# Kernel optimization log

Measured on AMD Instinct MI355X. Metric: run time of the kernel, lower is better.

The kernel has to match this reference:

```python
import jax, jax.numpy as jnp
import numpy as np

BN_EPS = 1e-5

def _bn(x, p):
    # p rows: gamma, beta, running_mean, running_var (eval-mode BatchNorm1d)
    g, b, m, v = p[0], p[1], p[2], p[3]
    return (x - m) * jax.lax.rsqrt(v + BN_EPS) * g + b

def setup_inputs() -> dict:
    key = jax.random.key(0)
    ks = iter(jax.random.split(key, 32))
    B, P, T, E, H = 16, 64, 8, 64, 64
    batch = B * P
    def w(shape, scale=0.1):
        return (jax.random.normal(next(ks), shape, dtype=jnp.float32) * scale)
    def bn_pack(d):
        k1, k2, k3, k4 = jax.random.split(next(ks), 4)
        gamma = 1.0 + 0.1 * jax.random.normal(k1, (d,), dtype=jnp.float32)
        beta = 0.1 * jax.random.normal(k2, (d,), dtype=jnp.float32)
        mean = 0.1 * jax.random.normal(k3, (d,), dtype=jnp.float32)
        var = 0.5 + jax.random.uniform(k4, (d,), dtype=jnp.float32)
        return jnp.stack([gamma, beta, mean, var], axis=0)
    return {
        "h_states": w((1, batch, H), 1.0),
        "end_pos": w((batch, 2), 1.0),
        "vx": w((T, batch), 1.0),
        "vy": w((T, batch), 1.0),
        "agent_type": jax.random.uniform(next(ks), (T, batch, 1), dtype=jnp.float32),
        "ws_w": w((2, E)), "ws_b": w((E,)),
        "wv_w": w((2, E)), "wv_b": w((E,)),
        "wa_w": w((6, E)), "wa_b": w((E,)),
        "att1_w": w((E, 1024)), "att1_b": w((1024,)), "att_bn1": bn_pack(1024),
        "att2_w": w((1024, 1)), "att2_b": w((1,)), "att_bn2": bn_pack(1),
        "pre1_w": w((E + H, 512)), "pre1_b": w((512,)), "pre_bn1": bn_pack(512),
        "pre2_w": w((512, 1024)), "pre2_b": w((1024,)), "pre_bn2": bn_pack(1024),
        "num_ped": P,
    }

def reference(h_states, end_pos, vx, vy, agent_type,
              ws_w, ws_b, wv_w, wv_b, wa_w, wa_b,
              att1_w, att1_b, att_bn1, att2_w, att2_b, att_bn2,
              pre1_w, pre1_b, pre_bn1, pre2_w, pre2_b, pre_bn2,
              num_ped):
    P = num_ped
    batch = end_pos.shape[0]
    B = batch // P  # uniform groups (seq_start_end = [(b*P, (b+1)*P)])
    H = h_states.shape[-1]
    h = h_states.reshape(batch, H).reshape(B, P, H)            # curr_hidden per group
    pos = end_pos.reshape(B, P, 2)
    # k = i*P + j: repeated row = pos[j], 'transposed' row = pos[i]
    rel = pos[:, None, :, :] - pos[:, :, None, :]               # [B, i, j, 2]
    rel_emb = rel @ ws_w + ws_b                                 # [B, i, j, E]
    # attention_mlp: Linear->BN->ReLU->Linear->BN->ReLU (make_mlp applies BN+act after every layer)
    a1 = jax.nn.relu(_bn(rel_emb @ att1_w + att1_b, att_bn1))   # [B, i, j, 1024]
    scores = jax.nn.relu(_bn(a1 @ att2_w + att2_b, att_bn2))    # [B, i, j, 1]
    # torch.softmax(scores, dim=1) on shape (n*n, 1): softmax over a singleton -> all ones
    aw = jax.nn.softmax(scores, axis=-1)
    # velocity embedding: computed in the original then discarded (dead code, kept for fidelity)
    vel = jnp.stack([vx[-1].reshape(B, P), vy[-1].reshape(B, P)], axis=-1)
    _vel_emb = vel @ wv_w + wv_b  # noqa: F841 (unused, matches original)
    # curr_agent_type.repeat(num_ped, 6): row k=i*P+j -> type[j] tiled to 6 features
    at6 = jnp.repeat(agent_type[0].reshape(B, P, 1), 6, axis=-1)  # [B, j, 6]
    at_emb = at6 @ wa_w + wa_b                                    # [B, j, E]
    feat_j = jnp.concatenate([h, at_emb], axis=-1)                # [B, j, H+E]
    weighted = jnp.broadcast_to(feat_j[:, None, :, :], (B, P, P, feat_j.shape[-1])) * (0.05 * aw)
    p1 = jax.nn.relu(_bn(weighted @ pre1_w + pre1_b, pre_bn1))    # [B, i, j, 512]
    p2 = jax.nn.relu(_bn(p1 @ pre2_w + pre2_b, pre_bn2))          # [B, i, j, 1024]
    pool = p2.max(axis=2)                                         # view(n,n,-1).max(1): max over j
    return pool.reshape(batch, -1)
```

## Files before the change

### kernel.cpp

```cpp
#include <hip/hip_runtime.h>
#include <hip/hip_bf16.h>

#define BN_EPS 1e-5f

typedef float f32x4 __attribute__((ext_vector_type(4)));
typedef __bf16 bfx8 __attribute__((ext_vector_type(8)));


__global__ __launch_bounds__(256) void k0_prep(
    const float* __restrict__ w2,
    const float* __restrict__ w1,
    const float* __restrict__ wa_w,
    const float* __restrict__ wa_b,
    __bf16* __restrict__ w2t,
    float* __restrict__ u_ws,
    float* __restrict__ v_ws)
{
    const int t = threadIdx.x;
    if (blockIdx.x < 128) {
        __shared__ float tile[64][69];
        const int bt  = blockIdx.x;
        const int kt0 = (bt & 7) * 64;
        const int n0  = (bt >> 3) * 64;
        #pragma unroll
        for (int i = 0; i < 4; ++i) {
            const int idx = t + i * 256;
            const int kk  = idx >> 4;
            const int nq  = (idx & 15) * 4;
            const f32x4 val = *(const f32x4*)&w2[(kt0 + kk) * 1024 + n0 + nq];
            #pragma unroll
            for (int j = 0; j < 4; ++j) tile[kk][nq + j] = val[j];
        }
        __syncthreads();
        #pragma unroll
        for (int i = 0; i < 2; ++i) {
            const int idx = t + i * 256;
            const int n   = idx >> 3;
            const int kq  = (idx & 7) * 8;
            bfx8 o;
            #pragma unroll
            for (int j = 0; j < 8; ++j) o[j] = (__bf16)tile[kq + j][n];
            *(bfx8*)&w2t[(n0 + n) * 512 + kt0 + kq] = o;
        }
    } else {
        __shared__ float Sl[64], Wbl[64];
        __shared__ float redu[4][64], redv[4][64];
        const int bu = blockIdx.x - 128;
        if (t < 64) {
            float s = 0.f;
            #pragma unroll
            for (int q = 0; q < 6; ++q) s += wa_w[q * 64 + t];
            Sl[t]  = s;
            Wbl[t] = wa_b[t];
        }
        __syncthreads();
        const int cl   = t & 63;
        const int eseg = t >> 6;
        const int c    = bu * 64 + cl;
        float pu = 0.f, pv = 0.f;
        for (int e = eseg * 16; e < eseg * 16 + 16; ++e) {
            const float w = w1[(64 + e) * 512 + c];
            pu = fmaf(Sl[e], w, pu);
            pv = fmaf(Wbl[e], w, pv);
        }
        redu[eseg][cl] = pu;
        redv[eseg][cl] = pv;
        __syncthreads();
        if (t < 64) {
            u_ws[bu * 64 + t] = redu[0][t] + redu[1][t] + redu[2][t] + redu[3][t];
            v_ws[bu * 64 + t] = redv[0][t] + redv[1][t] + redv[2][t] + redv[3][t];
        }
    }
}

__global__ __launch_bounds__(256) void k1_p1(
    const float* __restrict__ h,
    const float* __restrict__ at,
    const float* __restrict__ w1,
    const float* __restrict__ b1,
    const float* __restrict__ bn1,
    const float* __restrict__ u,
    const float* __restrict__ v,
    __bf16* __restrict__ p1b)
{
    __shared__ float x[4][64];
    const int r0 = blockIdx.x * 4;
    const int t  = threadIdx.x;
    x[t >> 6][t & 63] = 0.05f * h[(r0 + (t >> 6)) * 64 + (t & 63)];
    __syncthreads();

    float acc0[4] = {0.f, 0.f, 0.f, 0.f};
    float acc1[4] = {0.f, 0.f, 0.f, 0.f};
    #pragma unroll 8
    for (int k = 0; k < 64; ++k) {
        const float w0 = w1[k * 512 + t];
        const float wB = w1[k * 512 + t + 256];
        #pragma unroll
        for (int rr = 0; rr < 4; ++rr) {
            const float xv = x[rr][k];
            acc0[rr] = fmaf(xv, w0, acc0[rr]);
            acc1[rr] = fmaf(xv, wB, acc1[rr]);
        }
    }

    float at4[4];
    #pragma unroll
    for (int rr = 0; rr < 4; ++rr) at4[rr] = at[r0 + rr];

    #pragma unroll
    for (int which = 0; which < 2; ++which) {
        const int c = t + which * 256;
        const float uu = 0.05f * u[c];
        const float vv = fmaf(0.05f, v[c], b1[c]);
        const float g  = bn1[c];
        const float be = bn1[512 + c];
        const float mu = bn1[1024 + c];
        const float vr = bn1[1536 + c];
        const float s  = rsqrtf(vr + BN_EPS) * g;
        const float* acc = which ? acc1 : acc0;
        #pragma unroll
        for (int rr = 0; rr < 4; ++rr) {
            const float pre = acc[rr] + fmaf(at4[rr], uu, vv);
            const float val = fmaxf((pre - mu) * s + be, 0.0f);
            p1b[(r0 + rr) * 512 + c] = (__bf16)val;
        }
    }
}

__global__ __launch_bounds__(512) void k2_p2_pool(
    const __bf16* __restrict__ p1b,
    const __bf16* __restrict__ w2t,
    const float* __restrict__ b2,
    const float* __restrict__ bn2,
    float* __restrict__ out)
{
    const int cc = blockIdx.x;
    const int b  = blockIdx.y;
    const int t  = threadIdx.x;

    __shared__ __bf16 A_lds[64][136];
    __shared__ __bf16 B_lds[64][136];
    __shared__ float  red[4][64];

    const int wid  = t >> 6;
    const int lane = t & 63;
    const int mw   = wid >> 1;
    const int nw   = wid & 1;
    const int m0   = mw * 16;
    const int n0   = nw * 32;
    const int l15  = lane & 15;
    const int lhi  = lane >> 4;

    f32x4 acc[2] = {};

    for (int kt = 0; kt < 512; kt += 128) {
        #pragma unroll
        for (int i = 0; i < 2; ++i) {
            const int idx = t + i * 512;
            const int row = idx >> 4;
            const int kq  = (idx & 15) * 8;
            *(f32x4*)&A_lds[row][kq] =
                *(const f32x4*)&p1b[(b * 64 + row) * 512 + kt + kq];
            *(f32x4*)&B_lds[row][kq] =
                *(const f32x4*)&w2t[(cc * 64 + row) * 512 + kt + kq];
        }
        __syncthreads();

        #pragma unroll
        for (int ks = 0; ks < 4; ++ks) {
            const bfx8 a = *(const bfx8*)&A_lds[m0 + l15][ks * 32 + lhi * 8];
            #pragma unroll
            for (int f = 0; f < 2; ++f) {
                const bfx8 bb = *(const bfx8*)&B_lds[n0 + f * 16 + l15][ks * 32 + lhi * 8];
                acc[f] = __builtin_amdgcn_mfma_f32_16x16x32_bf16(a, bb, acc[f], 0, 0, 0);
            }
        }
        __syncthreads();
    }

    #pragma unroll
    for (int f = 0; f < 2; ++f) {
        const int cg   = cc * 64 + n0 + f * 16 + l15;
        const float s  = rsqrtf(bn2[3072 + cg] + BN_EPS) * bn2[cg];
        const float be = bn2[1024 + cg];
        const float mu = bn2[2048 + cg];
        const float bias = b2[cg];
        float mm = 0.f;
        #pragma unroll
        for (int r = 0; r < 3 + 1; ++r) {
            const float val = (acc[f][r] + bias - mu) * s + be;
            mm = fmaxf(mm, fmaxf(val, 0.f));
        }
        mm = fmaxf(mm, __shfl_xor(mm, 16));
        mm = fmaxf(mm, __shfl_xor(mm, 32));
        if (lane < 16) red[mw][n0 + f * 16 + lane] = mm;
    }
    __syncthreads();

    const int cl   = t & 63;
    const int iseg = t >> 6;
    const float pool = fmaxf(fmaxf(red[0][cl], red[1][cl]),
                             fmaxf(red[2][cl], red[3][cl]));
    const int ob = (b * 64 + iseg * 8) * 1024 + cc * 64 + cl;
    #pragma unroll
    for (int ii = 0; ii < 8; ++ii) out[ob + ii * 1024] = pool;
}

extern "C" void kernel_launch(void* const* d_in, const int* in_sizes, int n_in,
                              void* d_out, int out_size, void* d_ws, size_t ws_size,
                              hipStream_t stream) {
    const float* h    = (const float*)d_in[0];
    const float* at   = (const float*)d_in[4];
    const float* wa_w = (const float*)d_in[9];
    const float* wa_b = (const float*)d_in[10];
    const float* w1   = (const float*)d_in[17];
    const float* b1   = (const float*)d_in[18];
    const float* bn1  = (const float*)d_in[19];
    const float* w2   = (const float*)d_in[20];
    const float* b2   = (const float*)d_in[21];
    const float* bn2  = (const float*)d_in[22];

    char* ws = (char*)d_ws;
    __bf16* p1b = (__bf16*)ws;
    __bf16* w2t = (__bf16*)(ws + (1 << 20));
    float*  u   = (float*)(ws + (2 << 20));
    float*  v   = u + 512;
    float*  out = (float*)d_out;

    k0_prep<<<136, 256, 0, stream>>>(w2, w1, wa_w, wa_b, w2t, u, v);
    k1_p1<<<256, 256, 0, stream>>>(h, at, w1, b1, bn1, u, v, p1b);
    k2_p2_pool<<<dim3(16, 16), 512, 0, stream>>>(p1b, w2t, b2, bn2, out);
}
```

Before: 21.53 us.

## Fuse first MLP layer into pooled second GEMM kernel using MFMA

Merges the p1 computation into the p2+pool kernel. Each block now builds a bf16 64x128 input tile (scaled hidden plus agent-type embedding) and runs the first layer with bf16 MFMA against a transposed bf16 w1. The resulting p1 tile stays in LDS instead of going through global memory. The full 512-deep w2 slice is loaded into LDS in one pass, with its global loads issued early and held in registers. This removes one kernel launch and the p1 global round trip. In exchange, every column-chunk block recomputes layer 1 redundantly (16x duplication), LDS use is much larger, and layer 1 loses precision because its inputs are now bf16.

```diff
diff --git a/kernel.cpp b/kernel.cpp
--- a/kernel.cpp
+++ b/kernel.cpp
@@ -8,192 +8,193 @@
 
 
 __global__ __launch_bounds__(256) void k0_prep(
-    const float* __restrict__ w2,
-    const float* __restrict__ w1,
+    const float* __restrict__ w2, const float* __restrict__ w1,
+    __bf16* __restrict__ w2t, __bf16* __restrict__ w1t)
+{
+    __shared__ float tile[64][69];
+    const int t = threadIdx.x;
+    int kt0, n0, src_ld, dst_ld;
+    const float* src;
+    __bf16* dst;
+    if (blockIdx.x < 128) {
+        kt0 = (blockIdx.x & 7) * 64;  n0 = (blockIdx.x >> 3) * 64;
+        src = w2; src_ld = 1024; dst = w2t; dst_ld = 512;
+    } else {
+        const int bt = blockIdx.x - 128;
+        kt0 = (bt & 1) * 64;  n0 = (bt >> 1) * 64;
+        src = w1; src_ld = 512; dst = w1t; dst_ld = 128;
+    }
+    #pragma unroll
+    for (int i = 0; i < 4; ++i) {
+        const int idx = t + i * 256;
+        const int kk  = idx >> 4;
+        const int nq  = (idx & 15) * 4;
+        const f32x4 val = *(const f32x4*)&src[(size_t)(kt0 + kk) * src_ld + n0 + nq];
+        #pragma unroll
+        for (int j = 0; j < 4; ++j) tile[kk][nq + j] = val[j];
+    }
+    __syncthreads();
+    #pragma unroll
+    for (int i = 0; i < 2; ++i) {
+        const int idx = t + i * 256;
+        const int n   = idx >> 3;
+        const int kq  = (idx & 7) * 8;
+        bfx8 o;
+        #pragma unroll
+        for (int j = 0; j < 8; ++j) o[j] = (__bf16)tile[kq + j][n];
+        *(bfx8*)&dst[(size_t)(n0 + n) * dst_ld + kt0 + kq] = o;
+    }
+}
+
+__global__ __launch_bounds__(512, 2) void kmain(
+    const float* __restrict__ h,
+    const float* __restrict__ at,
     const float* __restrict__ wa_w,
     const float* __restrict__ wa_b,
-    __bf16* __restrict__ w2t,
-    float* __restrict__ u_ws,
-    float* __restrict__ v_ws)
-{
-    const int t = threadIdx.x;
-    if (blockIdx.x < 128) {
-        __shared__ float tile[64][69];
-        const int bt  = blockIdx.x;
-        const int kt0 = (bt & 7) * 64;
-        const int n0  = (bt >> 3) * 64;
-        #pragma unroll
-        for (int i = 0; i < 4; ++i) {
-            const int idx = t + i * 256;
-            const int kk  = idx >> 4;
-            const int nq  = (idx & 15) * 4;
-            const f32x4 val = *(const f32x4*)&w2[(kt0 + kk) * 1024 + n0 + nq];
-            #pragma unroll
-            for (int j = 0; j < 4; ++j) tile[kk][nq + j] = val[j];
-        }
-        __syncthreads();
-        #pragma unroll
-        for (int i = 0; i < 2; ++i) {
-            const int idx = t + i * 256;
-            const int n   = idx >> 3;
-            const int kq  = (idx & 7) * 8;
-            bfx8 o;
-            #pragma unroll
-            for (int j = 0; j < 8; ++j) o[j] = (__bf16)tile[kq + j][n];
-            *(bfx8*)&w2t[(n0 + n) * 512 + kt0 + kq] = o;
-        }
-    } else {
-        __shared__ float Sl[64], Wbl[64];
-        __shared__ float redu[4][64], redv[4][64];
-        const int bu = blockIdx.x - 128;
-        if (t < 64) {
-            float s = 0.f;
-            #pragma unroll
-            for (int q = 0; q < 6; ++q) s += wa_w[q * 64 + t];
-            Sl[t]  = s;
-            Wbl[t] = wa_b[t];
-        }
-        __syncthreads();
-        const int cl   = t & 63;
-        const int eseg = t >> 6;
-        const int c    = bu * 64 + cl;
-        float pu = 0.f, pv = 0.f;
-        for (int e = eseg * 16; e < eseg * 16 + 16; ++e) {
-            const float w = w1[(64 + e) * 512 + c];
-            pu = fmaf(Sl[e], w, pu);
-            pv = fmaf(Wbl[e], w, pv);
-        }
-        redu[eseg][cl] = pu;
-        redv[eseg][cl] = pv;
-        __syncthreads();
-        if (t < 64) {
-            u_ws[bu * 64 + t] = redu[0][t] + redu[1][t] + redu[2][t] + redu[3][t];
-            v_ws[bu * 64 + t] = redv[0][t] + redv[1][t] + redv[2][t] + redv[3][t];
-        }
-    }
-}
-
-__global__ __launch_bounds__(256) void k1_p1(
-    const float* __restrict__ h,
-    const float* __restrict__ at,
-    const float* __restrict__ w1,
+    const __bf16* __restrict__ w1t,
     const float* __restrict__ b1,
     const float* __restrict__ bn1,
-    const float* __restrict__ u,
-    const float* __restrict__ v,
-    __bf16* __restrict__ p1b)
-{
-    __shared__ float x[4][64];
-    const int r0 = blockIdx.x * 4;
-    const int t  = threadIdx.x;
-    x[t >> 6][t & 63] = 0.05f * h[(r0 + (t >> 6)) * 64 + (t & 63)];
-    __syncthreads();
-
-    float acc0[4] = {0.f, 0.f, 0.f, 0.f};
-    float acc1[4] = {0.f, 0.f, 0.f, 0.f};
-    #pragma unroll 8
-    for (int k = 0; k < 64; ++k) {
-        const float w0 = w1[k * 512 + t];
-        const float wB = w1[k * 512 + t + 256];
-        #pragma unroll
-        for (int rr = 0; rr < 4; ++rr) {
-            const float xv = x[rr][k];
-            acc0[rr] = fmaf(xv, w0, acc0[rr]);
-            acc1[rr] = fmaf(xv, wB, acc1[rr]);
-        }
-    }
-
-    float at4[4];
-    #pragma unroll
-    for (int rr = 0; rr < 4; ++rr) at4[rr] = at[r0 + rr];
-
-    #pragma unroll
-    for (int which = 0; which < 2; ++which) {
-        const int c = t + which * 256;
-        const float uu = 0.05f * u[c];
-        const float vv = fmaf(0.05f, v[c], b1[c]);
-        const float g  = bn1[c];
-        const float be = bn1[512 + c];
-        const float mu = bn1[1024 + c];
-        const float vr = bn1[1536 + c];
-        const float s  = rsqrtf(vr + BN_EPS) * g;
-        const float* acc = which ? acc1 : acc0;
-        #pragma unroll
-        for (int rr = 0; rr < 4; ++rr) {
-            const float pre = acc[rr] + fmaf(at4[rr], uu, vv);
-            const float val = fmaxf((pre - mu) * s + be, 0.0f);
-            p1b[(r0 + rr) * 512 + c] = (__bf16)val;
-        }
-    }
-}
-
-__global__ __launch_bounds__(512) void k2_p2_pool(
-    const __bf16* __restrict__ p1b,
     const __bf16* __restrict__ w2t,
     const float* __restrict__ b2,
     const float* __restrict__ bn2,
     float* __restrict__ out)
 {
-    const int cc = blockIdx.x;
-    const int b  = blockIdx.y;
-    const int t  = threadIdx.x;
-
-    __shared__ __bf16 A_lds[64][136];
-    __shared__ __bf16 B_lds[64][136];
-    __shared__ float  red[4][64];
-
+    const int cc   = blockIdx.x;
+    const int b    = blockIdx.y;
+    const int t    = threadIdx.x;
     const int wid  = t >> 6;
     const int lane = t & 63;
-    const int mw   = wid >> 1;
-    const int nw   = wid & 1;
-    const int m0   = mw * 16;
-    const int n0   = nw * 32;
     const int l15  = lane & 15;
     const int lhi  = lane >> 4;
 
-    f32x4 acc[2] = {};
-
-    for (int kt = 0; kt < 512; kt += 128) {
-        #pragma unroll
-        for (int i = 0; i < 2; ++i) {
-            const int idx = t + i * 512;
-            const int row = idx >> 4;
-            const int kq  = (idx & 15) * 8;
-            *(f32x4*)&A_lds[row][kq] =
-                *(const f32x4*)&p1b[(b * 64 + row) * 512 + kt + kq];
-            *(f32x4*)&B_lds[row][kq] =
-                *(const f32x4*)&w2t[(cc * 64 + row) * 512 + kt + kq];
-        }
-        __syncthreads();
-
-        #pragma unroll
-        for (int ks = 0; ks < 4; ++ks) {
-            const bfx8 a = *(const bfx8*)&A_lds[m0 + l15][ks * 32 + lhi * 8];
-            #pragma unroll
-            for (int f = 0; f < 2; ++f) {
-                const bfx8 bb = *(const bfx8*)&B_lds[n0 + f * 16 + l15][ks * 32 + lhi * 8];
-                acc[f] = __builtin_amdgcn_mfma_f32_16x16x32_bf16(a, bb, acc[f], 0, 0, 0);
+    __shared__ __bf16 x_lds[64][136];
+    __shared__ __bf16 p1_lds[64][520];
+    __shared__ __bf16 B2_lds[64][520];
+    __shared__ float  red[4][64];
+
+    f32x4 b2stage[8];
+    {
+        const char* base = (const char*)w2t + (size_t)(cc * 64) * 1024;
+        #pragma unroll
+        for (int i = 0; i < 8; ++i) {
+            const int n = i * 8 + wid;
+            b2stage[i] = *(const f32x4*)(base + (size_t)n * 1024 + lane * 16);
+        }
+    }
+
+    if (t < 64) {
+        float s = 0.f;
+        #pragma unroll
+        for (int q = 0; q < 6; ++q) s += wa_w[q * 64 + t];
+        red[0][t] = s;
+    }
+    __syncthreads();
+
+    #pragma unroll
+    for (int i = 0; i < 2; ++i) {
+        const int idx = t + i * 512;
+        const int rr  = idx >> 4;
+        const int cg  = (idx & 15) * 8;
+        bfx8 o;
+        if (cg < 64) {
+            const f32x4 v0 = *(const f32x4*)&h[(size_t)(b * 64 + rr) * 64 + cg];
+            const f32x4 v1 = *(const f32x4*)&h[(size_t)(b * 64 + rr) * 64 + cg + 4];
+            #pragma unroll
+            for (int j = 0; j < 4; ++j) {
+                o[j]     = (__bf16)(0.05f * v0[j]);
+                o[4 + j] = (__bf16)(0.05f * v1[j]);
             }
-        }
-        __syncthreads();
+        } else {
+            const float a = at[b * 64 + rr];
+            #pragma unroll
+            for (int j = 0; j < 8; ++j) {
+                const int e = cg - 64 + j;
+                o[j] = (__bf16)(0.05f * fmaf(a, red[0][e], wa_b[e]));
+            }
+        }
+        *(bfx8*)&x_lds[rr][cg] = o;
+    }
+    __syncthreads();
+
+    const int n0w = wid * 64;
+    bfx8 b1r[16];
+    #pragma unroll
+    for (int ks = 0; ks < 4; ++ks)
+        #pragma unroll
+        for (int nf = 0; nf < 4; ++nf)
+            b1r[ks * 4 + nf] = *(const bfx8*)(w1t +
+                (size_t)(n0w + nf * 16 + l15) * 128 + ks * 32 + lhi * 8);
+
+    f32x4 acc1[4][4] = {};
+    #pragma unroll
+    for (int ks = 0; ks < 4; ++ks) {
+        bfx8 a[4];
+        #pragma unroll
+        for (int mf = 0; mf < 4; ++mf)
+            a[mf] = *(const bfx8*)&x_lds[mf * 16 + l15][ks * 32 + lhi * 8];
+        #pragma unroll
+        for (int mf = 0; mf < 4; ++mf)
+            #pragma unroll
+            for (int nf = 0; nf < 4; ++nf)
+                acc1[mf][nf] = __builtin_amdgcn_mfma_f32_16x16x32_bf16(
+                    a[mf], b1r[ks * 4 + nf], acc1[mf][nf], 0, 0, 0);
+    }
+
+    #pragma unroll
+    for (int nf = 0; nf < 4; ++nf) {
+        const int c    = n0w + nf * 16 + l15;
+        const float s  = rsqrtf(bn1[1536 + c] + BN_EPS) * bn1[c];
+        const float be = bn1[512 + c];
+        const float mu = bn1[1024 + c];
+        const float bias = b1[c];
+        #pragma unroll
+        for (int mf = 0; mf < 4; ++mf)
+            #pragma unroll
+            for (int r = 0; r < 4; ++r) {
+                const float val =
+                    fmaxf((acc1[mf][nf][r] + bias - mu) * s + be, 0.f);
+                p1_lds[mf * 16 + lhi * 4 + r][c] = (__bf16)val;
+            }
+    }
+
+    #pragma unroll
+    for (int i = 0; i < 8; ++i) {
+        const int n = i * 8 + wid;
+        *(f32x4*)((char*)&B2_lds[0][0] + (size_t)n * 1040 + lane * 16) =
+            b2stage[i];
+    }
+    __syncthreads();
+
+    const int mw = wid >> 1;
+    const int nw = wid & 1;
+    f32x4 acc2[2] = {};
+    #pragma unroll
+    for (int ks = 0; ks < 16; ++ks) {
+        const bfx8 a = *(const bfx8*)&p1_lds[mw * 16 + l15][ks * 32 + lhi * 8];
+        #pragma unroll
+        for (int f = 0; f < 2; ++f) {
+            const bfx8 bb =
+                *(const bfx8*)&B2_lds[nw * 32 + f * 16 + l15][ks * 32 + lhi * 8];
+            acc2[f] = __builtin_amdgcn_mfma_f32_16x16x32_bf16(a, bb, acc2[f], 0, 0, 0);
+        }
     }
 
     #pragma unroll
     for (int f = 0; f < 2; ++f) {
-        const int cg   = cc * 64 + n0 + f * 16 + l15;
+        const int cg   = cc * 64 + nw * 32 + f * 16 + l15;
         const float s  = rsqrtf(bn2[3072 + cg] + BN_EPS) * bn2[cg];
         const float be = bn2[1024 + cg];
         const float mu = bn2[2048 + cg];
         const float bias = b2[cg];
         float mm = 0.f;
         #pragma unroll
-        for (int r = 0; r < 3 + 1; ++r) {
-            const float val = (acc[f][r] + bias - mu) * s + be;
+        for (int r = 0; r < 4; ++r) {
+            const float val = (acc2[f][r] + bias - mu) * s + be;
             mm = fmaxf(mm, fmaxf(val, 0.f));
         }
         mm = fmaxf(mm, __shfl_xor(mm, 16));
         mm = fmaxf(mm, __shfl_xor(mm, 32));
-        if (lane < 16) red[mw][n0 + f * 16 + lane] = mm;
+        if (lane < 16) red[mw][nw * 32 + f * 16 + lane] = mm;
     }
     __syncthreads();
 
@@ -221,13 +222,11 @@
     const float* bn2  = (const float*)d_in[22];
 
     char* ws = (char*)d_ws;
-    __bf16* p1b = (__bf16*)ws;
-    __bf16* w2t = (__bf16*)(ws + (1 << 20));
-    float*  u   = (float*)(ws + (2 << 20));
-    float*  v   = u + 512;
+    __bf16* w2t = (__bf16*)ws;
+    __bf16* w1t = (__bf16*)(ws + (1 << 20));
     float*  out = (float*)d_out;
 
-    k0_prep<<<136, 256, 0, stream>>>(w2, w1, wa_w, wa_b, w2t, u, v);
-    k1_p1<<<256, 256, 0, stream>>>(h, at, w1, b1, bn1, u, v, p1b);
-    k2_p2_pool<<<dim3(16, 16), 512, 0, stream>>>(p1b, w2t, b2, bn2, out);
+    k0_prep<<<144, 256, 0, stream>>>(w2, w1, w2t, w1t);
+    kmain<<<dim3(16, 16), 512, 0, stream>>>(h, at, wa_w, wa_b,
+                                            w1t, b1, bn1, w2t, b2, bn2, out);
 }
```

Result: faster. 21.06 us (-2.2%).
